# Performance work log

Measured on AMD Instinct MI355X. Metric: run time of the kernel, lower is better.

## Reference

```python
import math
import jax, jax.numpy as jnp
import numpy as np

T_NHEAD = 4
S_NHEAD = 4


def _ln(x, s, b, eps=1e-5):
    m = jnp.mean(x, axis=-1, keepdims=True)
    v = jnp.mean((x - m) ** 2, axis=-1, keepdims=True)
    return (x - m) / jnp.sqrt(v + eps) * s + b


def _pos_encoding(T, D):
    pos = jnp.arange(T, dtype=jnp.float32)[:, None]
    div = jnp.exp(jnp.arange(0, D, 2, dtype=jnp.float32) * (-math.log(10000.0) / D))
    pe = jnp.zeros((T, D), dtype=jnp.float32)
    pe = pe.at[:, 0::2].set(jnp.sin(pos * div))
    pe = pe.at[:, 1::2].set(jnp.cos(pos * div))
    return pe


def _forward(industry_ids, stock_features, market_features, emb_table, gate_w, gate_b,
             proj_w, proj_b, t_qw, t_kw, t_vw, t_ow, t_ob, t_nx_s, t_nx_b, t_nf_s, t_nf_b,
             t_f1w, t_f1b, t_f2w, t_f2b, s_qw, s_kw, s_vw, s_ow, s_ob, s_nx_s, s_nx_b,
             s_ni_s, s_ni_b, s_nf_s, s_nf_b, s_f1w, s_f1b, s_f2w, s_f2b, ta_w, dec_w, dec_b):
    N, T, F = stock_features.shape
    D = proj_w.shape[1]
    # industry embedding lookup
    ind_emb = emb_table[industry_ids]  # [N, E]
    # market gate (last timestep only), beta=1.0, scaled by d_output=d_feat
    mkt = market_features[:, -1, :]
    gate = F * jax.nn.softmax(mkt @ gate_w + gate_b, axis=-1)  # [N, F]
    x = stock_features * gate[:, None, :]
    # feature projection + positional encoding
    x = x @ proj_w + proj_b  # [N, T, D]
    x = x + _pos_encoding(T, D)
    # ---- TAttention (per-stock temporal self-attention) ----
    hd = D // T_NHEAD
    xs = _ln(x, t_nx_s, t_nx_b)
    q = (xs @ t_qw).reshape(N, T, T_NHEAD, hd)
    k = (xs @ t_kw).reshape(N, T, T_NHEAD, hd)
    v = (xs @ t_vw).reshape(N, T, T_NHEAD, hd)
    scores = jnp.einsum('nthd,nshd->nhts', q, k) / math.sqrt(hd)
    attn = jax.nn.softmax(scores, axis=-1)
    o = jnp.einsum('nhts,nshd->nthd', attn, v).reshape(N, T, D)
    xt = x + (o @ t_ow + t_ob)
    y = _ln(xt, t_nf_s, t_nf_b)
    xt = xt + (jax.nn.relu(y @ t_f1w + t_f1b) @ t_f2w + t_f2b)
    # ---- TemporalAttention (aggregate over time) ----
    h = xt @ ta_w  # [N, T, D]
    lam = jax.nn.softmax(jnp.einsum('ntd,nd->nt', h, h[:, -1, :]), axis=1)
    z = jnp.einsum('nt,ntd->nd', lam, xt)  # [N, D]
    # ---- SAttention (cross-stock attention over N) ----
    shd = D // S_NHEAD
    zs = _ln(z, s_nx_s, s_nx_b)
    ins = _ln(ind_emb, s_ni_s, s_ni_b)
    qk_in = jnp.concatenate([zs, ins], axis=-1)  # [N, D+E]
    sq = (qk_in @ s_qw).reshape(N, S_NHEAD, shd)
    sk = (qk_in @ s_kw).reshape(N, S_NHEAD, shd)
    sv = (zs @ s_vw).reshape(N, S_NHEAD, shd)
    sc = jnp.einsum('nhd,mhd->hnm', sq, sk) / math.sqrt(shd)
    sa = jax.nn.softmax(sc, axis=-1)
    so = jnp.einsum('hnm,mhd->nhd', sa, sv).reshape(N, D)
    zt = z + (so @ s_ow + s_ob)
    yn = _ln(zt, s_nf_s, s_nf_b)
    zt = zt + (jax.nn.relu(yn @ s_f1w + s_f1b) @ s_f2w + s_f2b)
    # decoder
    return zt @ dec_w + dec_b  # [N, 1]


def setup_inputs() -> dict:
    key = jax.random.key(0)
    ks = iter(jax.random.split(key, 64))
    N, T, F, M, E, D = 4096, 64, 158, 64, 32, 256
    def rn(shape, s=0.05):
        return jax.random.normal(next(ks), shape, dtype=jnp.float32) * s
    return dict(
        industry_ids=jax.random.randint(next(ks), (N,), 0, 256, dtype=jnp.int32),
        stock_features=rn((N, T, F), 1.0),
        market_features=rn((N, T, M), 1.0),
        emb_table=rn((256, E)),
        gate_w=rn((M, F)), gate_b=jnp.zeros((F,), jnp.float32),
        proj_w=rn((F, D)), proj_b=jnp.zeros((D,), jnp.float32),
        t_qw=rn((D, D)), t_kw=rn((D, D)), t_vw=rn((D, D)),
        t_ow=rn((D, D)), t_ob=jnp.zeros((D,), jnp.float32),
        t_nx_s=jnp.ones((D,), jnp.float32), t_nx_b=jnp.zeros((D,), jnp.float32),
        t_nf_s=jnp.ones((D,), jnp.float32), t_nf_b=jnp.zeros((D,), jnp.float32),
        t_f1w=rn((D, D)), t_f1b=jnp.zeros((D,), jnp.float32),
        t_f2w=rn((D, D)), t_f2b=jnp.zeros((D,), jnp.float32),
        s_qw=rn((D + E, D)), s_kw=rn((D + E, D)), s_vw=rn((D, D)),
        s_ow=rn((D, D)), s_ob=jnp.zeros((D,), jnp.float32),
        s_nx_s=jnp.ones((D,), jnp.float32), s_nx_b=jnp.zeros((D,), jnp.float32),
        s_ni_s=jnp.ones((E,), jnp.float32), s_ni_b=jnp.zeros((E,), jnp.float32),
        s_nf_s=jnp.ones((D,), jnp.float32), s_nf_b=jnp.zeros((D,), jnp.float32),
        s_f1w=rn((D, D)), s_f1b=jnp.zeros((D,), jnp.float32),
        s_f2w=rn((D, D)), s_f2b=jnp.zeros((D,), jnp.float32),
        ta_w=rn((D, D)),
        dec_w=rn((D, 1)), dec_b=jnp.zeros((1,), jnp.float32),
    )


def reference(industry_ids, stock_features, market_features, emb_table, gate_w, gate_b,
              proj_w, proj_b, t_qw, t_kw, t_vw, t_ow, t_ob, t_nx_s, t_nx_b, t_nf_s, t_nf_b,
              t_f1w, t_f1b, t_f2w, t_f2b, s_qw, s_kw, s_vw, s_ow, s_ob, s_nx_s, s_nx_b,
              s_ni_s, s_ni_b, s_nf_s, s_nf_b, s_f1w, s_f1b, s_f2w, s_f2b, ta_w, dec_w, dec_b):
    return _forward(industry_ids, stock_features, market_features, emb_table, gate_w, gate_b,
                    proj_w, proj_b, t_qw, t_kw, t_vw, t_ow, t_ob, t_nx_s, t_nx_b, t_nf_s, t_nf_b,
                    t_f1w, t_f1b, t_f2w, t_f2b, s_qw, s_kw, s_vw, s_ow, s_ob, s_nx_s, s_nx_b,
                    s_ni_s, s_ni_b, s_nf_s, s_nf_b, s_f1w, s_f1b, s_f2w, s_f2b, ta_w, dec_w, dec_b)
```

## Files before the change

kernel.cpp:

```cpp
#include <hip/hip_runtime.h>

typedef _Float16 f16;
typedef _Float16 f16x8 __attribute__((ext_vector_type(8)));
typedef _Float16 f16x4 __attribute__((ext_vector_type(4)));
typedef float    f32x4 __attribute__((ext_vector_type(4)));

#define MFMA32(a,b,c) __builtin_amdgcn_mfma_f32_16x16x32_f16((a),(b),(c),0,0,0)
#define MFMA16(a,b,c) __builtin_amdgcn_mfma_f32_16x16x16f16((a),(b),(c),0,0,0)

__device__ __forceinline__ f32x4 zero4() { f32x4 v = {0.f,0.f,0.f,0.f}; return v; }
#define ZERO44(A) { _Pragma("unroll") for (int z1=0;z1<4;++z1){ _Pragma("unroll") for (int z2=0;z2<4;++z2) A[z1][z2] = zero4(); } }

constexpr size_t OFF_PROJ = 0;
constexpr size_t OFF_QW  = 40960;
constexpr size_t OFF_KW  = 106496;
constexpr size_t OFF_VW  = 172032;
constexpr size_t OFF_OW  = 237568;
constexpr size_t OFF_F1  = 303104;
constexpr size_t OFF_F2  = 368640;
constexpr size_t OFF_TA  = 434176;
constexpr size_t OFF_SQW = 499712;
constexpr size_t OFF_SKW = 573440;
constexpr size_t OFF_SVW = 647168;
constexpr size_t OFF_SOW = 712704;
constexpr size_t OFF_SF1 = 778240;
constexpr size_t OFF_SF2 = 843776;
constexpr size_t W_ELEMS = 909312;
constexpr size_t PE_B  = W_ELEMS*2;
constexpr size_t Z_B   = PE_B  + 64*256*4;
constexpr size_t QK_B  = Z_B   + 4096ull*256*4;
constexpr size_t SQ_B  = QK_B  + 4096ull*288*2;
constexpr size_t SK_B  = SQ_B  + 4096ull*256*2;
constexpr size_t SVT_B = SK_B  + 4096ull*256*2;
constexpr size_t SO_B  = SVT_B + 4096ull*256*2;

struct PrepArgs {
  const float* src[14];
  int K[14]; int Kp[14]; int off[14];
};

__global__ void prep_kernel(PrepArgs a, f16* __restrict__ wbuf, float* __restrict__ pe) {
  int wsel = blockIdx.y;
  int tid = threadIdx.x;
  if (wsel < 14) {
    const float* S = a.src[wsel];
    int K = a.K[wsel], Kp = a.Kp[wsel];
    f16* D = wbuf + a.off[wsel];
    int n = blockIdx.x*4 + (tid & 3);
    for (int k = (tid >> 2); k < Kp; k += 64) {
      float v = (k < K) ? S[(size_t)k*256 + n] : 0.f;
      D[(size_t)n*Kp + k] = (f16)v;
    }
  } else {
    int idx = blockIdx.x*256 + tid;
    int t = idx >> 8, d = idx & 255, i = d >> 1;
    float div = expf((float)(2*i) * (-9.210340371976184f/256.f));
    float ang = (float)t * div;
    pe[idx] = (d & 1) ? cosf(ang) : sinf(ang);
  }
}

__device__ __forceinline__ void ln64(f16 (*src)[264], f16 (*dst)[264],
    const float* __restrict__ sc, const float* __restrict__ bi, int w, int lane) {
  int row = w*16 + (lane >> 2);
  int c0 = lane & 3;
  float s = 0.f, s2 = 0.f;
  for (int c = c0; c < 256; c += 4) { float v = (float)src[row][c]; s += v; s2 += v*v; }
  s  += __shfl_xor(s, 1);  s  += __shfl_xor(s, 2);
  s2 += __shfl_xor(s2, 1); s2 += __shfl_xor(s2, 2);
  float mean = s * (1.f/256.f);
  float var  = s2 * (1.f/256.f) - mean*mean;
  float rstd = rsqrtf(var + 1e-5f);
  for (int c = c0; c < 256; c += 4) {
    float v = ((float)src[row][c] - mean) * rstd * sc[c] + bi[c];
    dst[row][c] = (f16)v;
  }
}

template<int KSTEPS, int LDB>
__device__ __forceinline__ void gemm_ldsA(f16 (*A)[264], const f16* __restrict__ B,
                                          f32x4 (&acc)[4][4], int w, int l15, int g) {
  #pragma unroll
  for (int ks = 0; ks < KSTEPS; ++ks) {
    int kc = ks*32 + g*8;
    f16x8 av[4], bv[4];
    #pragma unroll
    for (int j = 0; j < 4; ++j) av[j] = *(const f16x8*)&A[j*16 + l15][kc];
    #pragma unroll
    for (int j = 0; j < 4; ++j) bv[j] = *(const f16x8*)(B + (size_t)(w*64 + j*16 + l15)*LDB + kc);
    #pragma unroll
    for (int mt = 0; mt < 4; ++mt) {
      #pragma unroll
      for (int nt = 0; nt < 4; ++nt)
        acc[mt][nt] = MFMA32(av[mt], bv[nt], acc[mt][nt]);
    }
  }
}

__device__ __forceinline__ void ffn_block(f16 (*res)[264], f16 (*y)[264], f16 (*u)[72],
    const f16* __restrict__ W1, const f16* __restrict__ W2,
    const float* __restrict__ b1, const float* __restrict__ b2,
    int w, int l15, int g) {
  f32x4 acc2[4][4]; ZERO44(acc2);
  for (int ch = 0; ch < 4; ++ch) {
    f32x4 ua[4];
    #pragma unroll
    for (int nt = 0; nt < 4; ++nt) ua[nt] = zero4();
    #pragma unroll
    for (int ks = 0; ks < 8; ++ks) {
      int kc = ks*32 + g*8;
      f16x8 av = *(const f16x8*)&y[w*16 + l15][kc];
      f16x8 bv[4];
      #pragma unroll
      for (int j = 0; j < 4; ++j) bv[j] = *(const f16x8*)(W1 + (size_t)(ch*64 + j*16 + l15)*256 + kc);
      #pragma unroll
      for (int nt = 0; nt < 4; ++nt) ua[nt] = MFMA32(av, bv[nt], ua[nt]);
    }
    __syncthreads();
    #pragma unroll
    for (int nt = 0; nt < 4; ++nt) {
      int col = nt*16 + l15;
      #pragma unroll
      for (int i = 0; i < 4; ++i) {
        float v = ua[nt][i] + b1[ch*64 + col];
        u[w*16 + g*4 + i][col] = (f16)fmaxf(v, 0.f);
      }
    }
    __syncthreads();
    #pragma unroll
    for (int ks = 0; ks < 2; ++ks) {
      int kc = ks*32 + g*8;
      f16x8 av[4], bv[4];
      #pragma unroll
      for (int j = 0; j < 4; ++j) av[j] = *(const f16x8*)&u[j*16 + l15][kc];
      #pragma unroll
      for (int j = 0; j < 4; ++j) bv[j] = *(const f16x8*)(W2 + (size_t)(w*64 + j*16 + l15)*256 + ch*64 + kc);
      #pragma unroll
      for (int mt = 0; mt < 4; ++mt) {
        #pragma unroll
        for (int nt = 0; nt < 4; ++nt)
          acc2[mt][nt] = MFMA32(av[mt], bv[nt], acc2[mt][nt]);
      }
    }
  }
  #pragma unroll
  for (int mt = 0; mt < 4; ++mt) {
    #pragma unroll
    for (int nt = 0; nt < 4; ++nt) {
      int col = w*64 + nt*16 + l15;
      #pragma unroll
      for (int i = 0; i < 4; ++i) {
        int row = mt*16 + g*4 + i;
        float v = (float)res[row][col] + acc2[mt][nt][i] + b2[col];
        res[row][col] = (f16)v;
      }
    }
  }
}

__global__ __launch_bounds__(256, 2) void temporal_kernel(
    const float* __restrict__ stock, const float* __restrict__ market,
    const float* __restrict__ gate_w, const float* __restrict__ gate_b,
    const float* __restrict__ proj_b, const float* __restrict__ t_ob,
    const float* __restrict__ t_nx_s, const float* __restrict__ t_nx_b,
    const float* __restrict__ t_nf_s, const float* __restrict__ t_nf_b,
    const float* __restrict__ t_f1b, const float* __restrict__ t_f2b,
    const f16* __restrict__ wbuf, const float* __restrict__ pe,
    float* __restrict__ zout)
{
  __shared__ __align__(16) f16 xb[64][264];
  __shared__ __align__(16) f16 bb[64][264];
  __shared__ __align__(16) f16 ub[64][72];
  __shared__ float gatev[160];
  __shared__ float mkt[64];
  __shared__ float red[66];

  const int tid = threadIdx.x;
  const int lane = tid & 63;
  const int w = tid >> 6;
  const int l15 = lane & 15;
  const int g = lane >> 4;
  const int n = blockIdx.x;

  if (tid < 64) mkt[tid] = market[(size_t)n*4096 + 63*64 + tid];
  __syncthreads();
  float logit = 0.f;
  if (tid < 158) {
    float acc = gate_b[tid];
    for (int m = 0; m < 64; ++m) acc += mkt[m] * gate_w[m*158 + tid];
    logit = acc;
  }
  if (tid < 160) gatev[tid] = (tid < 158) ? logit : -1e30f;
  __syncthreads();
  if (w == 0) {
    float v = fmaxf(gatev[lane], gatev[lane + 64]);
    if (lane < 32) v = fmaxf(v, gatev[lane + 128]);
    #pragma unroll
    for (int off = 32; off >= 1; off >>= 1) v = fmaxf(v, __shfl_xor(v, off));
    if (lane == 0) red[0] = v;
  }
  __syncthreads();
  float gmax = red[0];
  float ev = (tid < 158) ? __expf(logit - gmax) : 0.f;
  if (tid < 160) gatev[tid] = ev;
  __syncthreads();
  if (w == 0) {
    float v = gatev[lane] + gatev[lane + 64] + ((lane < 32) ? gatev[lane + 128] : 0.f);
    #pragma unroll
    for (int off = 32; off >= 1; off >>= 1) v += __shfl_xor(v, off);
    if (lane == 0) red[1] = v;
  }
  __syncthreads();
  const float grs = 158.f / red[1];

  for (int idx = tid; idx < 64*158; idx += 256) {
    int t = idx / 158, f = idx - t*158;
    bb[t][f] = (f16)(stock[(size_t)n*(64*158) + idx] * (gatev[f] * grs));
  }
  if (tid < 128) bb[tid >> 1][158 + (tid & 1)] = (f16)0.f;
  __syncthreads();

  {
    f32x4 acc[4][4]; ZERO44(acc);
    gemm_ldsA<5,160>(bb, wbuf + OFF_PROJ, acc, w, l15, g);
    #pragma unroll
    for (int mt = 0; mt < 4; ++mt) {
      #pragma unroll
      for (int nt = 0; nt < 4; ++nt) {
        int col = w*64 + nt*16 + l15;
        #pragma unroll
        for (int i = 0; i < 4; ++i) {
          int row = mt*16 + g*4 + i;
          xb[row][col] = (f16)(acc[mt][nt][i] + proj_b[col] + pe[row*256 + col]);
        }
      }
    }
  }
  __syncthreads();
  ln64(xb, bb, t_nx_s, t_nx_b, w, lane);
  __syncthreads();

  {
    const int h = w;
    f16x4 qf[4][4], kf[4][4], vf[4][4];
    {
      f32x4 acc[4][4]; ZERO44(acc);
      #pragma unroll
      for (int ks = 0; ks < 8; ++ks) {
        int kc = ks*32 + g*8;
        f16x8 xv[4], wv[4];
        #pragma unroll
        for (int j = 0; j < 4; ++j) xv[j] = *(const f16x8*)&bb[j*16 + l15][kc];
        #pragma unroll
        for (int j = 0; j < 4; ++j) wv[j] = *(const f16x8*)(wbuf + OFF_QW + (size_t)(h*64 + j*16 + l15)*256 + kc);
        #pragma unroll
        for (int md = 0; md < 4; ++md) {
          #pragma unroll
          for (int nt = 0; nt < 4; ++nt) acc[md][nt] = MFMA32(wv[md], xv[nt], acc[md][nt]);
        }
      }
      #pragma unroll
      for (int md = 0; md < 4; ++md) { 
        #pragma unroll
        for (int nt = 0; nt < 4; ++nt) { 
          #pragma unroll
          for (int i = 0; i < 4; ++i) qf[md][nt][i] = (f16)(acc[md][nt][i] * 0.125f);
        }
      }
    }
    {
      f32x4 acc[4][4]; ZERO44(acc);
      #pragma unroll
      for (int ks = 0; ks < 8; ++ks) {
        int kc = ks*32 + g*8;
        f16x8 xv[4], wv[4];
        #pragma unroll
        for (int j = 0; j < 4; ++j) xv[j] = *(const f16x8*)&bb[j*16 + l15][kc];
        #pragma unroll
        for (int j = 0; j < 4; ++j) wv[j] = *(const f16x8*)(wbuf + OFF_KW + (size_t)(h*64 + j*16 + l15)*256 + kc);
        #pragma unroll
        for (int md = 0; md < 4; ++md) {
          #pragma unroll
          for (int nt = 0; nt < 4; ++nt) acc[md][nt] = MFMA32(wv[md], xv[nt], acc[md][nt]);
        }
      }
      #pragma unroll
      for (int md = 0; md < 4; ++md) { 
        #pragma unroll
        for (int nt = 0; nt < 4; ++nt) { 
          #pragma unroll
          for (int i = 0; i < 4; ++i) kf[md][nt][i] = (f16)acc[md][nt][i];
        }
      }
    }
    {
      f32x4 acc[4][4]; ZERO44(acc);
      #pragma unroll
      for (int ks = 0; ks < 8; ++ks) {
        int kc = ks*32 + g*8;
        f16x8 xv[4], wv[4];
        #pragma unroll
        for (int j = 0; j < 4; ++j) xv[j] = *(const f16x8*)&bb[j*16 + l15][kc];
        #pragma unroll
        for (int j = 0; j < 4; ++j) wv[j] = *(const f16x8*)(wbuf + OFF_VW + (size_t)(h*64 + j*16 + l15)*256 + kc);
        #pragma unroll
        for (int ms = 0; ms < 4; ++ms) {
          #pragma unroll
          for (int nd = 0; nd < 4; ++nd) acc[ms][nd] = MFMA32(xv[ms], wv[nd], acc[ms][nd]);
        }
      }
      #pragma unroll
      for (int ms = 0; ms < 4; ++ms) { 
        #pragma unroll
        for (int nd = 0; nd < 4; ++nd) { 
          #pragma unroll
          for (int i = 0; i < 4; ++i) vf[ms][nd][i] = (f16)acc[ms][nd][i];
        }
      }
    }
    f32x4 sacc[4][4]; ZERO44(sacc);
    #pragma unroll
    for (int kd = 0; kd < 4; ++kd) {
      #pragma unroll
      for (int ms = 0; ms < 4; ++ms) {
        #pragma unroll
        for (int nt = 0; nt < 4; ++nt)
          sacc[ms][nt] = MFMA16(kf[kd][ms], qf[kd][nt], sacc[ms][nt]);
      }
    }
    f16x4 pf[4][4];
    #pragma unroll
    for (int nt = 0; nt < 4; ++nt) {
      float mx = -1e30f;
      #pragma unroll
      for (int ms = 0; ms < 4; ++ms) {
        #pragma unroll
        for (int i = 0; i < 4; ++i) mx = fmaxf(mx, sacc[ms][nt][i]);
      }
      mx = fmaxf(mx, __shfl_xor(mx, 16));
      mx = fmaxf(mx, __shfl_xor(mx, 32));
      float sm = 0.f;
      #pragma unroll
      for (int ms = 0; ms < 4; ++ms) {
        #pragma unroll
        for (int i = 0; i < 4; ++i) { float e = __expf(sacc[ms][nt][i] - mx); sacc[ms][nt][i] = e; sm += e; }
      }
      sm += __shfl_xor(sm, 16);
      sm += __shfl_xor(sm, 32);
      float r = 1.f / sm;
      #pragma unroll
      for (int ms = 0; ms < 4; ++ms) {
        #pragma unroll
        for (int i = 0; i < 4; ++i) pf[ms][nt][i] = (f16)(sacc[ms][nt][i] * r);
      }
    }
    f32x4 oacc[4][4]; ZERO44(oacc);
    #pragma unroll
    for (int ks = 0; ks < 4; ++ks) {
      #pragma unroll
      for (int md = 0; md < 4; ++md) {
        #pragma unroll
        for (int nt = 0; nt < 4; ++nt)
          oacc[md][nt] = MFMA16(vf[ks][md], pf[ks][nt], oacc[md][nt]);
      }
    }
    __syncthreads();
    #pragma unroll
    for (int md = 0; md < 4; ++md) {
      #pragma unroll
      for (int nt = 0; nt < 4; ++nt) {
        int t = nt*16 + l15;
        f16x4 ov;
        #pragma unroll
        for (int i = 0; i < 4; ++i) ov[i] = (f16)oacc[md][nt][i];
        *(f16x4*)&bb[t][h*64 + md*16 + g*4] = ov;
      }
    }
  }
  __syncthreads();

  {
    f32x4 acc[4][4]; ZERO44(acc);
    gemm_ldsA<8,256>(bb, wbuf + OFF_OW, acc, w, l15, g);
    #pragma unroll
    for (int mt = 0; mt < 4; ++mt) {
      #pragma unroll
      for (int nt = 0; nt < 4; ++nt) {
        int col = w*64 + nt*16 + l15;
        #pragma unroll
        for (int i = 0; i < 4; ++i) {
          int row = mt*16 + g*4 + i;
          xb[row][col] = (f16)((float)xb[row][col] + acc[mt][nt][i] + t_ob[col]);
        }
      }
    }
  }
  __syncthreads();
  ln64(xb, bb, t_nf_s, t_nf_b, w, lane);
  __syncthreads();
  ffn_block(xb, bb, ub, wbuf + OFF_F1, wbuf + OFF_F2, t_f1b, t_f2b, w, l15, g);
  __syncthreads();

  {
    f32x4 acc[4][4]; ZERO44(acc);
    gemm_ldsA<8,256>(xb, wbuf + OFF_TA, acc, w, l15, g);
    #pragma unroll
    for (int mt = 0; mt < 4; ++mt) {
      #pragma unroll
      for (int nt = 0; nt < 4; ++nt) {
        int col = w*64 + nt*16 + l15;
        #pragma unroll
        for (int i = 0; i < 4; ++i) bb[mt*16 + g*4 + i][col] = (f16)acc[mt][nt][i];
      }
    }
  }
  __syncthreads();

  {
    int row = w*16 + (lane >> 2);
    int c0 = lane & 3;
    float dt = 0.f;
    for (int c = c0; c < 256; c += 4) dt += (float)bb[row][c] * (float)bb[63][c];
    dt += __shfl_xor(dt, 1); dt += __shfl_xor(dt, 2);
    if (c0 == 0) red[2 + row] = dt;
  }
  __syncthreads();
  if (tid < 64) {
    float v = red[2 + tid];
    float mx = v;
    #pragma unroll
    for (int off = 32; off >= 1; off >>= 1) mx = fmaxf(mx, __shfl_xor(mx, off));
    float e = __expf(v - mx);
    float sm = e;
    #pragma unroll
    for (int off = 32; off >= 1; off >>= 1) sm += __shfl_xor(sm, off);
    red[2 + tid] = e / sm;
  }
  __syncthreads();
  {
    float za = 0.f;
    #pragma unroll 8
    for (int t = 0; t < 64; ++t) za += red[2 + t] * (float)xb[t][tid];
    zout[(size_t)n*256 + tid] = za;
  }
}

__global__ __launch_bounds__(256) void qkin_kernel(
    const float* __restrict__ z, const int* __restrict__ ids,
    const float* __restrict__ emb,
    const float* __restrict__ s_nx_s, const float* __restrict__ s_nx_b,
    const float* __restrict__ s_ni_s, const float* __restrict__ s_ni_b,
    f16* __restrict__ qk)
{
  int lane = threadIdx.x & 63;
  int w = threadIdx.x >> 6;
  int r = blockIdx.x*4 + w;
  const float* zr = z + (size_t)r*256;
  float v[4]; float s = 0.f, s2 = 0.f;
  #pragma unroll
  for (int j = 0; j < 4; ++j) { v[j] = zr[lane*4 + j]; s += v[j]; s2 += v[j]*v[j]; }
  #pragma unroll
  for (int off = 32; off >= 1; off >>= 1) { s += __shfl_xor(s, off); s2 += __shfl_xor(s2, off); }
  float mean = s*(1.f/256.f);
  float rstd = rsqrtf(s2*(1.f/256.f) - mean*mean + 1e-5f);
  f16* q = qk + (size_t)r*288;
  #pragma unroll
  for (int j = 0; j < 4; ++j) {
    int c = lane*4 + j;
    q[c] = (f16)((v[j] - mean)*rstd*s_nx_s[c] + s_nx_b[c]);
  }
  int id = ids[r];
  float e = (lane < 32) ? emb[id*32 + lane] : 0.f;
  float es = e, es2 = e*e;
  #pragma unroll
  for (int off = 16; off >= 1; off >>= 1) { es += __shfl_xor(es, off); es2 += __shfl_xor(es2, off); }
  if (lane < 32) {
    float m2 = es*(1.f/32.f);
    float rs2 = rsqrtf(es2*(1.f/32.f) - m2*m2 + 1e-5f);
    q[256 + lane] = (f16)((e - m2)*rs2*s_ni_s[lane] + s_ni_b[lane]);
  }
}

__global__ __launch_bounds__(256) void sqk_kernel(const f16* __restrict__ qk,
    const f16* __restrict__ wbuf, f16* __restrict__ sq, f16* __restrict__ sk)
{
  const int tid = threadIdx.x, lane = tid & 63, w = tid >> 6, l15 = lane & 15, g = lane >> 4;
  const int isk = blockIdx.y;
  const f16* W = wbuf + (isk ? OFF_SKW : OFF_SQW);
  f16* out = isk ? sk : sq;
  const float scale = isk ? 1.f : 0.125f;
  const int r0 = blockIdx.x*64;
  f32x4 acc[4][4]; ZERO44(acc);
  #pragma unroll
  for (int ks = 0; ks < 9; ++ks) {
    int kc = ks*32 + g*8;
    f16x8 av[4], bv[4];
    #pragma unroll
    for (int j = 0; j < 4; ++j) av[j] = *(const f16x8*)(qk + (size_t)(r0 + j*16 + l15)*288 + kc);
    #pragma unroll
    for (int j = 0; j < 4; ++j) bv[j] = *(const f16x8*)(W + (size_t)(w*64 + j*16 + l15)*288 + kc);
    #pragma unroll
    for (int mt = 0; mt < 4; ++mt) {
      #pragma unroll
      for (int nt = 0; nt < 4; ++nt) acc[mt][nt] = MFMA32(av[mt], bv[nt], acc[mt][nt]);
    }
  }
  #pragma unroll
  for (int mt = 0; mt < 4; ++mt) {
    #pragma unroll
    for (int nt = 0; nt < 4; ++nt) {
      int col = w*64 + nt*16 + l15;
      #pragma unroll
      for (int i = 0; i < 4; ++i)
        out[(size_t)(r0 + mt*16 + g*4 + i)*256 + col] = (f16)(acc[mt][nt][i]*scale);
    }
  }
}

__global__ __launch_bounds__(256) void svt_kernel(const f16* __restrict__ qk,
    const f16* __restrict__ wbuf, f16* __restrict__ svT)
{
  const int tid = threadIdx.x, lane = tid & 63, w = tid >> 6, l15 = lane & 15, g = lane >> 4;
  const int k0 = blockIdx.x*64;
  f32x4 acc[4][4]; ZERO44(acc);
  #pragma unroll
  for (int ks = 0; ks < 8; ++ks) {
    int kc = ks*32 + g*8;
    f16x8 av[4], bv[4];
    #pragma unroll
    for (int j = 0; j < 4; ++j) av[j] = *(const f16x8*)(wbuf + OFF_SVW + (size_t)(w*64 + j*16 + l15)*256 + kc);
    #pragma unroll
    for (int j = 0; j < 4; ++j) bv[j] = *(const f16x8*)(qk + (size_t)(k0 + j*16 + l15)*288 + kc);
    #pragma unroll
    for (int md = 0; md < 4; ++md) {
      #pragma unroll
      for (int nk = 0; nk < 4; ++nk) acc[md][nk] = MFMA32(av[md], bv[nk], acc[md][nk]);
    }
  }
  #pragma unroll
  for (int md = 0; md < 4; ++md) {
    #pragma unroll
    for (int nk = 0; nk < 4; ++nk) {
      int key = k0 + nk*16 + l15;
      #pragma unroll
      for (int i = 0; i < 4; ++i)
        svT[(size_t)(w*64 + md*16 + g*4 + i)*4096 + key] = (f16)acc[md][nk][i];
    }
  }
}

__global__ __launch_bounds__(256) void xattn_kernel(const f16* __restrict__ sq,
    const f16* __restrict__ sk, const f16* __restrict__ svT, f16* __restrict__ so)
{
  const int lane = threadIdx.x & 63, w = threadIdx.x >> 6, l15 = lane & 15, g = lane >> 4;
  const int h = blockIdx.y;
  const int q0 = blockIdx.x*64 + w*16;
  const f16* qp = sq + (size_t)q0*256 + h*64;
  f16x8 qf0 = *(const f16x8*)(qp + (size_t)l15*256 + g*8);
  f16x8 qf1 = *(const f16x8*)(qp + (size_t)l15*256 + 32 + g*8);
  f32x4 oacc[4];
  #pragma unroll
  for (int md = 0; md < 4; ++md) oacc[md] = zero4();
  float mrun = -1e30f, lrun = 0.f;
  for (int kt = 0; kt < 64; ++kt) {
    const f16* kp = sk + (size_t)kt*64*256 + h*64;
    f32x4 sacc[4];
    #pragma unroll
    for (int mt = 0; mt < 4; ++mt) sacc[mt] = zero4();
    #pragma unroll
    for (int mt = 0; mt < 4; ++mt) {
      f16x8 k0f = *(const f16x8*)(kp + (size_t)(mt*16 + l15)*256 + g*8);
      f16x8 k1f = *(const f16x8*)(kp + (size_t)(mt*16 + l15)*256 + 32 + g*8);
      sacc[mt] = MFMA32(k0f, qf0, sacc[mt]);
      sacc[mt] = MFMA32(k1f, qf1, sacc[mt]);
    }
    float tmax = -1e30f;
    #pragma unroll
    for (int mt = 0; mt < 4; ++mt) {
      #pragma unroll
      for (int i = 0; i < 4; ++i) tmax = fmaxf(tmax, sacc[mt][i]);
    }
    tmax = fmaxf(tmax, __shfl_xor(tmax, 16));
    tmax = fmaxf(tmax, __shfl_xor(tmax, 32));
    float mnew = fmaxf(mrun, tmax);
    float corr = __expf(mrun - mnew);
    float ts = 0.f;
    #pragma unroll
    for (int mt = 0; mt < 4; ++mt) {
      #pragma unroll
      for (int i = 0; i < 4; ++i) { float e = __expf(sacc[mt][i] - mnew); sacc[mt][i] = e; ts += e; }
    }
    ts += __shfl_xor(ts, 16);
    ts += __shfl_xor(ts, 32);
    lrun = lrun*corr + ts;
    mrun = mnew;
    f16x4 pf[4];
    #pragma unroll
    for (int mt = 0; mt < 4; ++mt) {
      #pragma unroll
      for (int i = 0; i < 4; ++i) pf[mt][i] = (f16)sacc[mt][i];
    }
    #pragma unroll
    for (int md = 0; md < 4; ++md) {
      #pragma unroll
      for (int i = 0; i < 4; ++i) oacc[md][i] *= corr;
    }
    const f16* vp = svT + (size_t)h*64*4096 + kt*64;
    #pragma unroll
    for (int ks = 0; ks < 4; ++ks) {
      #pragma unroll
      for (int md = 0; md < 4; ++md) {
        f16x4 vf = *(const f16x4*)(vp + (size_t)(md*16 + l15)*4096 + ks*16 + g*4);
        oacc[md] = MFMA16(vf, pf[ks], oacc[md]);
      }
    }
  }
  float rinv = 1.f / lrun;
  #pragma unroll
  for (int md = 0; md < 4; ++md) {
    f16x4 ov;
    #pragma unroll
    for (int i = 0; i < 4; ++i) ov[i] = (f16)(oacc[md][i]*rinv);
    *(f16x4*)(so + (size_t)(q0 + l15)*256 + h*64 + md*16 + g*4) = ov;
  }
}

__global__ __launch_bounds__(256, 2) void final_kernel(
    const f16* __restrict__ so, const float* __restrict__ z,
    const f16* __restrict__ wbuf,
    const float* __restrict__ s_ob,
    const float* __restrict__ s_nf_s, const float* __restrict__ s_nf_b,
    const float* __restrict__ s_f1b, const float* __restrict__ s_f2b,
    const float* __restrict__ dec_w, const float* __restrict__ dec_b,
    float* __restrict__ out)
{
  __shared__ __align__(16) f16 zb[64][264];
  __shared__ __align__(16) f16 yb[64][264];
  __shared__ __align__(16) f16 ub[64][72];
  const int tid = threadIdx.x, lane = tid & 63, w = tid >> 6, l15 = lane & 15, g = lane >> 4;
  const int r0 = blockIdx.x*64;
  {
    f32x4 acc[4][4]; ZERO44(acc);
    #pragma unroll
    for (int ks = 0; ks < 8; ++ks) {
      int kc = ks*32 + g*8;
      f16x8 av[4], bv[4];
      #pragma unroll
      for (int j = 0; j < 4; ++j) av[j] = *(const f16x8*)(so + (size_t)(r0 + j*16 + l15)*256 + kc);
      #pragma unroll
      for (int j = 0; j < 4; ++j) bv[j] = *(const f16x8*)(wbuf + OFF_SOW + (size_t)(w*64 + j*16 + l15)*256 + kc);
      #pragma unroll
      for (int mt = 0; mt < 4; ++mt) {
        #pragma unroll
        for (int nt = 0; nt < 4; ++nt) acc[mt][nt] = MFMA32(av[mt], bv[nt], acc[mt][nt]);
      }
    }
    #pragma unroll
    for (int mt = 0; mt < 4; ++mt) {
      #pragma unroll
      for (int nt = 0; nt < 4; ++nt) {
        int col = w*64 + nt*16 + l15;
        #pragma unroll
        for (int i = 0; i < 4; ++i) {
          int row = mt*16 + g*4 + i;
          zb[row][col] = (f16)(z[(size_t)(r0 + row)*256 + col] + acc[mt][nt][i] + s_ob[col]);
        }
      }
    }
  }
  __syncthreads();
  ln64(zb, yb, s_nf_s, s_nf_b, w, lane);
  __syncthreads();
  ffn_block(zb, yb, ub, wbuf + OFF_SF1, wbuf + OFF_SF2, s_f1b, s_f2b, w, l15, g);
  __syncthreads();
  {
    int row = w*16 + (lane >> 2), c0 = lane & 3;
    float dt = 0.f;
    for (int c = c0; c < 256; c += 4) dt += (float)zb[row][c]*dec_w[c];
    dt += __shfl_xor(dt, 1); dt += __shfl_xor(dt, 2);
    if (c0 == 0) out[r0 + row] = dt + dec_b[0];
  }
}

extern "C" void kernel_launch(void* const* d_in, const int* in_sizes, int n_in,
                              void* d_out, int out_size, void* d_ws, size_t ws_size,
                              hipStream_t stream)
{
  const int*   ids    = (const int*)  d_in[0];
  const float* stock  = (const float*)d_in[1];
  const float* market = (const float*)d_in[2];
  const float* emb    = (const float*)d_in[3];
  const float* gate_w = (const float*)d_in[4];
  const float* gate_b = (const float*)d_in[5];

  char* ws = (char*)d_ws;
  f16*   wbuf = (f16*)ws;
  float* pe   = (float*)(ws + PE_B);
  float* zbuf = (float*)(ws + Z_B);
  f16*   qk   = (f16*)(ws + QK_B);
  f16*   sq   = (f16*)(ws + SQ_B);
  f16*   sk   = (f16*)(ws + SK_B);
  f16*   svT  = (f16*)(ws + SVT_B);
  f16*   so   = (f16*)(ws + SO_B);

  PrepArgs pa;
  const int srcIdx[14] = {6,8,9,10,11,17,19,36,21,22,23,24,32,34};
  const int Ks[14]   = {158,256,256,256,256,256,256,256,288,288,256,256,256,256};
  const int Kps[14]  = {160,256,256,256,256,256,256,256,288,288,256,256,256,256};
  const int offs[14] = {(int)OFF_PROJ,(int)OFF_QW,(int)OFF_KW,(int)OFF_VW,(int)OFF_OW,
                        (int)OFF_F1,(int)OFF_F2,(int)OFF_TA,(int)OFF_SQW,(int)OFF_SKW,
                        (int)OFF_SVW,(int)OFF_SOW,(int)OFF_SF1,(int)OFF_SF2};
  for (int i = 0; i < 14; ++i) {
    pa.src[i] = (const float*)d_in[srcIdx[i]];
    pa.K[i] = Ks[i]; pa.Kp[i] = Kps[i]; pa.off[i] = offs[i];
  }

  prep_kernel<<<dim3(64,15), dim3(256), 0, stream>>>(pa, wbuf, pe);
  temporal_kernel<<<dim3(4096), dim3(256), 0, stream>>>(
      stock, market, gate_w, gate_b,
      (const float*)d_in[7],  (const float*)d_in[12],
      (const float*)d_in[13], (const float*)d_in[14],
      (const float*)d_in[15], (const float*)d_in[16],
      (const float*)d_in[18], (const float*)d_in[20],
      wbuf, pe, zbuf);
  qkin_kernel<<<dim3(1024), dim3(256), 0, stream>>>(
      zbuf, ids, emb,
      (const float*)d_in[26], (const float*)d_in[27],
      (const float*)d_in[28], (const float*)d_in[29], qk);
  sqk_kernel<<<dim3(64,2), dim3(256), 0, stream>>>(qk, wbuf, sq, sk);
  svt_kernel<<<dim3(64), dim3(256), 0, stream>>>(qk, wbuf, svT);
  xattn_kernel<<<dim3(64,4), dim3(256), 0, stream>>>(sq, sk, svT, so);
  final_kernel<<<dim3(64), dim3(256), 0, stream>>>(
      so, zbuf, wbuf,
      (const float*)d_in[25], (const float*)d_in[30], (const float*)d_in[31],
      (const float*)d_in[33], (const float*)d_in[35],
      (const float*)d_in[37], (const float*)d_in[38], (float*)d_out);
}
```

Before: 1.267 ms.

## Keep temporal residual in registers, share one LDS buffer, vectorize layernorm

The temporal kernel drops the second 64x264 f16 LDS buffer and keeps the residual stream in per-thread registers (xres). This shrinks shared memory so three blocks can fit per CU instead of two. LayerNorm and the dot-product loops now use 8-wide f16 vector LDS loads, and the FFN is inlined with a per-wave row split plus extra barriers so the single buffer can be reused in place. The cost is more register pressure under the tighter launch bound, which risks spills, plus extra synchronisation.

Result: slower. 2.060 ms (+62.5%).

```diff
diff --git a/kernel.cpp b/kernel.cpp
--- a/kernel.cpp
+++ b/kernel.cpp
@@ -60,20 +60,30 @@
   }
 }
 
-__device__ __forceinline__ void ln64(f16 (*src)[264], f16 (*dst)[264],
+__device__ __forceinline__ void ln64v(f16 (*src)[264], f16 (*dst)[264],
     const float* __restrict__ sc, const float* __restrict__ bi, int w, int lane) {
   int row = w*16 + (lane >> 2);
   int c0 = lane & 3;
+  f16x8 v[8];
   float s = 0.f, s2 = 0.f;
-  for (int c = c0; c < 256; c += 4) { float v = (float)src[row][c]; s += v; s2 += v*v; }
+  #pragma unroll
+  for (int j = 0; j < 8; ++j) {
+    v[j] = *(const f16x8*)&src[row][j*32 + c0*8];
+    #pragma unroll
+    for (int e = 0; e < 8; ++e) { float f = (float)v[j][e]; s += f; s2 += f*f; }
+  }
   s  += __shfl_xor(s, 1);  s  += __shfl_xor(s, 2);
   s2 += __shfl_xor(s2, 1); s2 += __shfl_xor(s2, 2);
   float mean = s * (1.f/256.f);
-  float var  = s2 * (1.f/256.f) - mean*mean;
-  float rstd = rsqrtf(var + 1e-5f);
-  for (int c = c0; c < 256; c += 4) {
-    float v = ((float)src[row][c] - mean) * rstd * sc[c] + bi[c];
-    dst[row][c] = (f16)v;
+  float rstd = rsqrtf(s2 * (1.f/256.f) - mean*mean + 1e-5f);
+  #pragma unroll
+  for (int j = 0; j < 8; ++j) {
+    int c = j*32 + c0*8;
+    f16x8 o;
+    #pragma unroll
+    for (int e = 0; e < 8; ++e)
+      o[e] = (f16)(((float)v[j][e] - mean) * rstd * sc[c+e] + bi[c+e]);
+    *(f16x8*)&dst[row][c] = o;
   }
 }
 
@@ -158,7 +168,7 @@
   }
 }
 
-__global__ __launch_bounds__(256, 2) void temporal_kernel(
+__global__ __launch_bounds__(256, 3) void temporal_kernel(
     const float* __restrict__ stock, const float* __restrict__ market,
     const float* __restrict__ gate_w, const float* __restrict__ gate_b,
     const float* __restrict__ proj_b, const float* __restrict__ t_ob,
@@ -168,8 +178,7 @@
     const f16* __restrict__ wbuf, const float* __restrict__ pe,
     float* __restrict__ zout)
 {
-  __shared__ __align__(16) f16 xb[64][264];
-  __shared__ __align__(16) f16 bb[64][264];
+  __shared__ __align__(16) f16 B[64][264];
   __shared__ __align__(16) f16 ub[64][72];
   __shared__ float gatev[160];
   __shared__ float mkt[64];
@@ -182,6 +191,8 @@
   const int g = lane >> 4;
   const int n = blockIdx.x;
 
+  f16x4 xres[4][4];
+
   if (tid < 64) mkt[tid] = market[(size_t)n*4096 + 63*64 + tid];
   __syncthreads();
   float logit = 0.f;
@@ -215,14 +226,15 @@
 
   for (int idx = tid; idx < 64*158; idx += 256) {
     int t = idx / 158, f = idx - t*158;
-    bb[t][f] = (f16)(stock[(size_t)n*(64*158) + idx] * (gatev[f] * grs));
-  }
-  if (tid < 128) bb[tid >> 1][158 + (tid & 1)] = (f16)0.f;
+    B[t][f] = (f16)(stock[(size_t)n*(64*158) + idx] * (gatev[f] * grs));
+  }
+  if (tid < 128) B[tid >> 1][158 + (tid & 1)] = (f16)0.f;
   __syncthreads();
 
   {
     f32x4 acc[4][4]; ZERO44(acc);
-    gemm_ldsA<5,160>(bb, wbuf + OFF_PROJ, acc, w, l15, g);
+    gemm_ldsA<5,160>(B, wbuf + OFF_PROJ, acc, w, l15, g);
+    __syncthreads();
     #pragma unroll
     for (int mt = 0; mt < 4; ++mt) {
       #pragma unroll
@@ -231,13 +243,15 @@
         #pragma unroll
         for (int i = 0; i < 4; ++i) {
           int row = mt*16 + g*4 + i;
-          xb[row][col] = (f16)(acc[mt][nt][i] + proj_b[col] + pe[row*256 + col]);
-        }
-      }
-    }
-  }
-  __syncthreads();
-  ln64(xb, bb, t_nx_s, t_nx_b, w, lane);
+          float vv = acc[mt][nt][i] + proj_b[col] + pe[row*256 + col];
+          xres[mt][nt][i] = (f16)vv;
+          B[row][col] = (f16)vv;
+        }
+      }
+    }
+  }
+  __syncthreads();
+  ln64v(B, B, t_nx_s, t_nx_b, w, lane);
   __syncthreads();
 
   {
@@ -250,7 +264,7 @@
         int kc = ks*32 + g*8;
         f16x8 xv[4], wv[4];
         #pragma unroll
-        for (int j = 0; j < 4; ++j) xv[j] = *(const f16x8*)&bb[j*16 + l15][kc];
+        for (int j = 0; j < 4; ++j) xv[j] = *(const f16x8*)&B[j*16 + l15][kc];
         #pragma unroll
         for (int j = 0; j < 4; ++j) wv[j] = *(const f16x8*)(wbuf + OFF_QW + (size_t)(h*64 + j*16 + l15)*256 + kc);
         #pragma unroll
@@ -260,9 +274,9 @@
         }
       }
       #pragma unroll
-      for (int md = 0; md < 4; ++md) { 
-        #pragma unroll
-        for (int nt = 0; nt < 4; ++nt) { 
+      for (int md = 0; md < 4; ++md) {
+        #pragma unroll
+        for (int nt = 0; nt < 4; ++nt) {
           #pragma unroll
           for (int i = 0; i < 4; ++i) qf[md][nt][i] = (f16)(acc[md][nt][i] * 0.125f);
         }
@@ -275,7 +289,7 @@
         int kc = ks*32 + g*8;
         f16x8 xv[4], wv[4];
         #pragma unroll
-        for (int j = 0; j < 4; ++j) xv[j] = *(const f16x8*)&bb[j*16 + l15][kc];
+        for (int j = 0; j < 4; ++j) xv[j] = *(const f16x8*)&B[j*16 + l15][kc];
         #pragma unroll
         for (int j = 0; j < 4; ++j) wv[j] = *(const f16x8*)(wbuf + OFF_KW + (size_t)(h*64 + j*16 + l15)*256 + kc);
         #pragma unroll
@@ -285,9 +299,9 @@
         }
       }
       #pragma unroll
-      for (int md = 0; md < 4; ++md) { 
-        #pragma unroll
-        for (int nt = 0; nt < 4; ++nt) { 
+      for (int md = 0; md < 4; ++md) {
+        #pragma unroll
+        for (int nt = 0; nt < 4; ++nt) {
           #pragma unroll
           for (int i = 0; i < 4; ++i) kf[md][nt][i] = (f16)acc[md][nt][i];
         }
@@ -300,7 +314,7 @@
         int kc = ks*32 + g*8;
         f16x8 xv[4], wv[4];
         #pragma unroll
-        for (int j = 0; j < 4; ++j) xv[j] = *(const f16x8*)&bb[j*16 + l15][kc];
+        for (int j = 0; j < 4; ++j) xv[j] = *(const f16x8*)&B[j*16 + l15][kc];
         #pragma unroll
         for (int j = 0; j < 4; ++j) wv[j] = *(const f16x8*)(wbuf + OFF_VW + (size_t)(h*64 + j*16 + l15)*256 + kc);
         #pragma unroll
@@ -310,9 +324,9 @@
         }
       }
       #pragma unroll
-      for (int ms = 0; ms < 4; ++ms) { 
-        #pragma unroll
-        for (int nd = 0; nd < 4; ++nd) { 
+      for (int ms = 0; ms < 4; ++ms) {
+        #pragma unroll
+        for (int nd = 0; nd < 4; ++nd) {
           #pragma unroll
           for (int i = 0; i < 4; ++i) vf[ms][nd][i] = (f16)acc[ms][nd][i];
         }
@@ -373,7 +387,7 @@
         f16x4 ov;
         #pragma unroll
         for (int i = 0; i < 4; ++i) ov[i] = (f16)oacc[md][nt][i];
-        *(f16x4*)&bb[t][h*64 + md*16 + g*4] = ov;
+        *(f16x4*)&B[t][h*64 + md*16 + g*4] = ov;
       }
     }
   }
@@ -381,7 +395,8 @@
 
   {
     f32x4 acc[4][4]; ZERO44(acc);
-    gemm_ldsA<8,256>(bb, wbuf + OFF_OW, acc, w, l15, g);
+    gemm_ldsA<8,256>(B, wbuf + OFF_OW, acc, w, l15, g);
+    __syncthreads();
     #pragma unroll
     for (int mt = 0; mt < 4; ++mt) {
       #pragma unroll
@@ -390,27 +405,88 @@
         #pragma unroll
         for (int i = 0; i < 4; ++i) {
           int row = mt*16 + g*4 + i;
-          xb[row][col] = (f16)((float)xb[row][col] + acc[mt][nt][i] + t_ob[col]);
-        }
-      }
-    }
-  }
-  __syncthreads();
-  ln64(xb, bb, t_nf_s, t_nf_b, w, lane);
-  __syncthreads();
-  ffn_block(xb, bb, ub, wbuf + OFF_F1, wbuf + OFF_F2, t_f1b, t_f2b, w, l15, g);
+          float vv = (float)xres[mt][nt][i] + acc[mt][nt][i] + t_ob[col];
+          xres[mt][nt][i] = (f16)vv;
+          B[row][col] = (f16)vv;
+        }
+      }
+    }
+  }
+  __syncthreads();
+  ln64v(B, B, t_nf_s, t_nf_b, w, lane);
+  __syncthreads();
+
+  {
+    f32x4 acc2[4][4]; ZERO44(acc2);
+    for (int ch = 0; ch < 4; ++ch) {
+      f32x4 ua[4];
+      #pragma unroll
+      for (int nt = 0; nt < 4; ++nt) ua[nt] = zero4();
+      #pragma unroll
+      for (int ks = 0; ks < 8; ++ks) {
+        int kc = ks*32 + g*8;
+        f16x8 av = *(const f16x8*)&B[w*16 + l15][kc];
+        f16x8 bv[4];
+        #pragma unroll
+        for (int j = 0; j < 4; ++j) bv[j] = *(const f16x8*)(wbuf + OFF_F1 + (size_t)(ch*64 + j*16 + l15)*256 + kc);
+        #pragma unroll
+        for (int nt = 0; nt < 4; ++nt) ua[nt] = MFMA32(av, bv[nt], ua[nt]);
+      }
+      __syncthreads();
+      #pragma unroll
+      for (int nt = 0; nt < 4; ++nt) {
+        int col = nt*16 + l15;
+        #pragma unroll
+        for (int i = 0; i < 4; ++i) {
+          float v = ua[nt][i] + t_f1b[ch*64 + col];
+          ub[w*16 + g*4 + i][col] = (f16)fmaxf(v, 0.f);
+        }
+      }
+      __syncthreads();
+      #pragma unroll
+      for (int ks = 0; ks < 2; ++ks) {
+        int kc = ks*32 + g*8;
+        f16x8 av[4], bv[4];
+        #pragma unroll
+        for (int j = 0; j < 4; ++j) av[j] = *(const f16x8*)&ub[j*16 + l15][kc];
+        #pragma unroll
+        for (int j = 0; j < 4; ++j) bv[j] = *(const f16x8*)(wbuf + OFF_F2 + (size_t)(w*64 + j*16 + l15)*256 + ch*64 + kc);
+        #pragma unroll
+        for (int mt = 0; mt < 4; ++mt) {
+          #pragma unroll
+          for (int nt = 0; nt < 4; ++nt)
+            acc2[mt][nt] = MFMA32(av[mt], bv[nt], acc2[mt][nt]);
+        }
+      }
+    }
+    #pragma unroll
+    for (int mt = 0; mt < 4; ++mt) {
+      #pragma unroll
+      for (int nt = 0; nt < 4; ++nt) {
+        int col = w*64 + nt*16 + l15;
+        #pragma unroll
+        for (int i = 0; i < 4; ++i) {
+          int row = mt*16 + g*4 + i;
+          float vv = (float)xres[mt][nt][i] + acc2[mt][nt][i] + t_f2b[col];
+          xres[mt][nt][i] = (f16)vv;
+          B[row][col] = (f16)vv;
+        }
+      }
+    }
+  }
   __syncthreads();
 
   {
     f32x4 acc[4][4]; ZERO44(acc);
-    gemm_ldsA<8,256>(xb, wbuf + OFF_TA, acc, w, l15, g);
+    gemm_ldsA<8,256>(B, wbuf + OFF_TA, acc, w, l15, g);
+    __syncthreads();
     #pragma unroll
     for (int mt = 0; mt < 4; ++mt) {
       #pragma unroll
       for (int nt = 0; nt < 4; ++nt) {
         int col = w*64 + nt*16 + l15;
         #pragma unroll
-        for (int i = 0; i < 4; ++i) bb[mt*16 + g*4 + i][col] = (f16)acc[mt][nt][i];
+        for (int i = 0; i < 4; ++i) B[mt*16 + g*4 + i][col] = (f16)acc[mt][nt][i];
       }
     }
   }
@@ -420,7 +496,13 @@
     int row = w*16 + (lane >> 2);
     int c0 = lane & 3;
     float dt = 0.f;
-    for (int c = c0; c < 256; c += 4) dt += (float)bb[row][c] * (float)bb[63][c];
+    #pragma unroll
+    for (int j = 0; j < 8; ++j) {
+      f16x8 va = *(const f16x8*)&B[row][j*32 + c0*8];
+      f16x8 vb = *(const f16x8*)&B[63][j*32 + c0*8];
+      #pragma unroll
+      for (int e = 0; e < 8; ++e) dt += (float)va[e] * (float)vb[e];
+    }
     dt += __shfl_xor(dt, 1); dt += __shfl_xor(dt, 2);
     if (c0 == 0) red[2 + row] = dt;
   }
@@ -438,10 +520,26 @@
   }
   __syncthreads();
   {
-    float za = 0.f;
-    #pragma unroll 8
-    for (int t = 0; t < 64; ++t) za += red[2 + t] * (float)xb[t][tid];
-    zout[(size_t)n*256 + tid] = za;
+    float zacc[4] = {0.f, 0.f, 0.f, 0.f};
+    #pragma unroll
+    for (int mt = 0; mt < 4; ++mt) {
+      #pragma unroll
+      for (int i = 0; i < 4; ++i) {
+        float l = red[2 + mt*16 + g*4 + i];
+        #pragma unroll
+        for (int nt = 0; nt < 4; ++nt) zacc[nt] += l * (float)xres[mt][nt][i];
+      }
+    }
+    #pragma unroll
+    for (int nt = 0; nt < 4; ++nt) {
+      zacc[nt] += __shfl_xor(zacc[nt], 16);
+      zacc[nt] += __shfl_xor(zacc[nt], 32);
+    }
+    if (g == 0) {
+      #pragma unroll
+      for (int nt = 0; nt < 4; ++nt)
+        zout[(size_t)n*256 + w*64 + nt*16 + l15] = zacc[nt];
+    }
   }
 }
 
@@ -669,14 +767,19 @@
     }
   }
   __syncthreads();
-  ln64(zb, yb, s_nf_s, s_nf_b, w, lane);
+  ln64v(zb, yb, s_nf_s, s_nf_b, w, lane);
   __syncthreads();
   ffn_block(zb, yb, ub, wbuf + OFF_SF1, wbuf + OFF_SF2, s_f1b, s_f2b, w, l15, g);
   __syncthreads();
   {
     int row = w*16 + (lane >> 2), c0 = lane & 3;
     float dt = 0.f;
-    for (int c = c0; c < 256; c += 4) dt += (float)zb[row][c]*dec_w[c];
+    #pragma unroll
+    for (int j = 0; j < 8; ++j) {
+      f16x8 va = *(const f16x8*)&zb[row][j*32 + c0*8];
+      #pragma unroll
+      for (int e = 0; e < 8; ++e) dt += (float)va[e]*dec_w[j*32 + c0*8 + e];
+    }
     dt += __shfl_xor(dt, 1); dt += __shfl_xor(dt, 2);
     if (c0 == 0) out[r0 + row] = dt + dec_b[0];
   }
```
